# Kernel optimization log

Measured on AMD Instinct MI355X. Metric: run time of the kernel, lower is better.

The kernel has to match this reference:

```python
import jax, jax.numpy as jnp
import numpy as np

TILE = 128

def _dequant(Wq, scales, zeros):
    # Wq: [out, n_cols] int codes; scales/zeros: [n_tiles, out]
    n_cols = Wq.shape[1]
    tids = jnp.arange(n_cols) // TILE            # tile id per column
    s = scales[tids].T                           # [out, n_cols]
    z = zeros[tids].T                            # [out, n_cols]
    return (Wq.astype(jnp.float32) - z) * s

def setup_inputs() -> dict:
    key = jax.random.key(0)
    ks = jax.random.split(key, 9)
    B, IN, OUT = 256, 8192, 8192
    n_high, n_low = 2048, 6144
    nt_hi, nt_lo = 16, 48
    x = jax.random.normal(ks[0], (B, IN), dtype=jnp.float32)
    W_high_q = jax.random.randint(ks[1], (OUT, n_high), 0, 64, dtype=jnp.int32)
    W_low_q = jax.random.randint(ks[2], (OUT, n_low), 0, 32, dtype=jnp.int32)
    scales_high = jax.random.uniform(ks[3], (nt_hi, OUT), dtype=jnp.float32, minval=0.001, maxval=0.05)
    zeros_high = jax.random.normal(ks[4], (nt_hi, OUT), dtype=jnp.float32) * 16.0
    scales_low = jax.random.uniform(ks[5], (nt_lo, OUT), dtype=jnp.float32, minval=0.001, maxval=0.05)
    zeros_low = jax.random.normal(ks[6], (nt_lo, OUT), dtype=jnp.float32) * 8.0
    bias = jax.random.normal(ks[7], (OUT,), dtype=jnp.float32) * 0.02
    col_indices = jax.random.permutation(ks[8], IN).astype(jnp.int32)
    return {"x": x, "W_high_q": W_high_q, "W_low_q": W_low_q,
            "scales_high": scales_high, "zeros_high": zeros_high,
            "scales_low": scales_low, "zeros_low": zeros_low,
            "bias": bias, "col_indices": col_indices}

def reference(x, W_high_q, W_low_q, scales_high, zeros_high,
              scales_low, zeros_low, bias, col_indices):
    # Dequantize both precision regions (per-tile affine: (q - zero) * scale)
    W_high = _dequant(W_high_q, scales_high, zeros_high)   # [out, n_high]
    W_low = _dequant(W_low_q, scales_low, zeros_low)       # [out, n_low]
    W_perm = jnp.concatenate([W_high, W_low], axis=1)      # [out, in]
    # y = x @ W.T where W[:, col_indices] = W_perm  <=>  gather x columns instead
    x_perm = x[:, col_indices]                             # [B, in]
    return x_perm @ W_perm.T + bias[None, :]
```

## Files before the change

### kernel.cpp

```cpp
#include <hip/hip_runtime.h>
#include <stdint.h>


#define IN_DIM 8192
#define OUT_DIM 8192
#define BDIM 256
#define NH 2048
#define NL 6144
#define BN 64
#define BK 32
#define KSPLIT 4
#define KSEG (IN_DIM / KSPLIT)
#define NSTEP (KSEG / BK)
#define NTILE (KSEG / 128)

#define XOFF 0
#define WOFF 32768
#define SCOFF 40960
#define ZSOFF 45056

typedef __bf16 bf16x8 __attribute__((ext_vector_type(8)));
typedef float f32x4 __attribute__((ext_vector_type(4)));

__device__ __forceinline__ unsigned short bfbits(float f) {
  union { float f; unsigned int u; } v; v.f = f;
  unsigned int u = v.u;
  u += 0x7fffu + ((u >> 16) & 1u);
  return (unsigned short)(u >> 16);
}
__device__ __forceinline__ unsigned int pk2(float a, float b) {
  return (unsigned int)bfbits(a) | ((unsigned int)bfbits(b) << 16);
}

extern "C" __global__ void gather_k(const float* __restrict__ x,
                                    const int* __restrict__ ci,
                                    unsigned short* __restrict__ xp) {
  int i4 = blockIdx.x * blockDim.x + threadIdx.x;
  int b = i4 >> 11;
  int k4 = (i4 & 2047) << 2;
  int4 c = *(const int4*)(ci + k4);
  const float* xr = x + (size_t)b * IN_DIM;
  uint2 st;
  st.x = pk2(xr[c.x], xr[c.y]);
  st.y = pk2(xr[c.z], xr[c.w]);
  *(uint2*)(xp + (size_t)b * IN_DIM + k4) = st;
}

extern "C" __global__ __launch_bounds__(256, 2)
void gemm_k(const unsigned short* __restrict__ xp,
            const int* __restrict__ Whq, const int* __restrict__ Wlq,
            const float* __restrict__ sh, const float* __restrict__ zh,
            const float* __restrict__ sl, const float* __restrict__ zl,
            const float* __restrict__ bias,
            float* __restrict__ outp,
            int use_atomic)
{
  __shared__ char smem[49152];
  const int t = threadIdx.x;
  const int lane = t & 63;
  const int wv = t >> 6;
  const int kh = blockIdx.y;
  const int n0 = blockIdx.x * BN;
  const int l15 = lane & 15;
  const int g4 = lane >> 4;

  const int xr = t >> 2;
  const int xc = (t & 3) ^ (xr & 3);
  const unsigned short* xg0 = xp + (size_t)xr * IN_DIM + (size_t)kh * KSEG + xc * 8;

  const int wcol = t >> 2;
  const int wm = t & 3;
  const int* wb0 = (kh == 0) ? (Whq + (size_t)(n0 + wcol) * NH)
                             : (Wlq + (size_t)(n0 + wcol) * NL + (size_t)(kh - 1) * KSEG);
  const float* sbase = ((kh == 0) ? sh : sl + (size_t)(kh - 1) * NTILE * OUT_DIM) + n0;
  const float* zbase = ((kh == 0) ? zh : zl + (size_t)(kh - 1) * NTILE * OUT_DIM) + n0;

  f32x4 acc[4][4];
  {
    float bvj[4];
    #pragma unroll
    for (int j = 0; j < 4; ++j)
      bvj[j] = (kh == 0) ? bias[n0 + j * 16 + l15] : 0.f;
    #pragma unroll
    for (int i = 0; i < 4; ++i)
      #pragma unroll
      for (int j = 0; j < 4; ++j) {
        acc[i][j][0] = bvj[j]; acc[i][j][1] = bvj[j];
        acc[i][j][2] = bvj[j]; acc[i][j][3] = bvj[j];
      }
  }

  auto stage_x = [&](int bx, int s) {
    const unsigned short* g = xg0 + s * BK;
    char* lb = smem + XOFF + bx * 16384 + wv * 1024;
    #pragma unroll
    for (int r = 0; r < 4; ++r)
      __builtin_amdgcn_global_load_lds(
          (const __attribute__((address_space(1))) void*)(g + (size_t)r * 64 * IN_DIM),
          (__attribute__((address_space(3))) void*)(lb + r * 4096), 16, 0, 0);
  };
  auto wload = [&](int4& a, int4& b, int s) {
    const int* p = wb0 + s * BK + wm * 8;
    a = *(const int4*)p;
    b = *(const int4*)(p + 4);
  };
  auto wdeq = [&](int bx, int4 a, int4 b, int s) {
    int tl = s >> 2;
    float sc = *(const float*)(smem + SCOFF + (tl * 64 + wcol) * 4);
    float zs = *(const float*)(smem + ZSOFF + (tl * 64 + wcol) * 4);
    uint4 d;
    d.x = pk2((float)a.x * sc - zs, (float)a.y * sc - zs);
    d.y = pk2((float)a.z * sc - zs, (float)a.w * sc - zs);
    d.z = pk2((float)b.x * sc - zs, (float)b.y * sc - zs);
    d.w = pk2((float)b.z * sc - zs, (float)b.w * sc - zs);
    *(uint4*)(smem + WOFF + bx * 4096 + wcol * 64 + ((wm ^ (wcol & 3)) * 16)) = d;
  };
  auto compute = [&](int bx) {
    const char* xb = smem + XOFF + bx * 16384;
    const char* wbuf = smem + WOFF + bx * 4096;
    bf16x8 a[4], b[4];
    #pragma unroll
    for (int i = 0; i < 4; ++i) {
      int row = wv * 64 + i * 16 + l15;
      int ch = g4 ^ (row & 3);
      a[i] = *(const bf16x8*)(xb + row * 64 + ch * 16);
    }
    #pragma unroll
    for (int j = 0; j < 4; ++j) {
      int col = j * 16 + l15;
      int ch = g4 ^ (col & 3);
      b[j] = *(const bf16x8*)(wbuf + col * 64 + ch * 16);
    }
    #pragma unroll
    for (int i = 0; i < 4; ++i)
      #pragma unroll
      for (int j = 0; j < 4; ++j)
        acc[i][j] = __builtin_amdgcn_mfma_f32_16x16x32_bf16(a[i], b[j], acc[i][j], 0, 0, 0);
  };

  #pragma unroll
  for (int r = 0; r < 4; ++r) {
    int p = t + r * 256;
    float s_ = sbase[(size_t)(p >> 6) * OUT_DIM + (p & 63)];
    float z_ = zbase[(size_t)(p >> 6) * OUT_DIM + (p & 63)];
    *(float*)(smem + SCOFF + p * 4) = s_;
    *(float*)(smem + ZSOFF + p * 4) = z_ * s_;
  }
  stage_x(0, 0);
  int4 qa0, qa1, qb0, qb1;
  wload(qa0, qa1, 0);
  wload(qb0, qb1, 1);
  __syncthreads();
  wdeq(0, qa0, qa1, 0);
  asm volatile("s_waitcnt lgkmcnt(0)" ::: "memory");
  __builtin_amdgcn_s_barrier();

  #pragma unroll 1
  for (int it = 0; it < 31; ++it) {
    const int s = it * 2;
    __builtin_amdgcn_sched_barrier(0);
    stage_x(1, s + 1);
    __builtin_amdgcn_sched_barrier(0);
    wload(qa0, qa1, s + 2);
    __builtin_amdgcn_sched_barrier(0);
    compute(0);
    wdeq(1, qb0, qb1, s + 1);
    asm volatile("s_waitcnt vmcnt(2) lgkmcnt(0)" ::: "memory");
    __builtin_amdgcn_s_barrier();
    __builtin_amdgcn_sched_barrier(0);
    stage_x(0, s + 2);
    __builtin_amdgcn_sched_barrier(0);
    wload(qb0, qb1, s + 3);
    __builtin_amdgcn_sched_barrier(0);
    compute(1);
    wdeq(0, qa0, qa1, s + 2);
    asm volatile("s_waitcnt vmcnt(2) lgkmcnt(0)" ::: "memory");
    __builtin_amdgcn_s_barrier();
  }
  __builtin_amdgcn_sched_barrier(0);
  stage_x(1, 63);
  __builtin_amdgcn_sched_barrier(0);
  compute(0);
  wdeq(1, qb0, qb1, 63);
  asm volatile("s_waitcnt vmcnt(0) lgkmcnt(0)" ::: "memory");
  __builtin_amdgcn_s_barrier();
  compute(1);

  if (use_atomic) {
    #pragma unroll
    for (int i = 0; i < 4; ++i) {
      int row0 = wv * 64 + i * 16 + g4 * 4;
      #pragma unroll
      for (int j = 0; j < 4; ++j) {
        int col = n0 + j * 16 + l15;
        #pragma unroll
        for (int r = 0; r < 4; ++r)
          atomicAdd(&outp[(size_t)(row0 + r) * OUT_DIM + col], acc[i][j][r]);
      }
    }
  } else {
    float* pp = outp + (size_t)kh * ((size_t)BDIM * OUT_DIM);
    #pragma unroll
    for (int i = 0; i < 4; ++i) {
      int row0 = wv * 64 + i * 16 + g4 * 4;
      #pragma unroll
      for (int j = 0; j < 4; ++j) {
        int col = n0 + j * 16 + l15;
        #pragma unroll
        for (int r = 0; r < 4; ++r)
          pp[(size_t)(row0 + r) * OUT_DIM + col] = acc[i][j][r];
      }
    }
  }
}

extern "C" __global__ void reduce_k(const float* __restrict__ part,
                                    float* __restrict__ out) {
  int i4 = blockIdx.x * blockDim.x + threadIdx.x;
  size_t off = (size_t)i4 * 4;
  const size_t S = (size_t)BDIM * OUT_DIM;
  float4 p0 = *(const float4*)(part + off);
  float4 p1 = *(const float4*)(part + off + S);
  float4 p2 = *(const float4*)(part + off + 2 * S);
  float4 p3 = *(const float4*)(part + off + 3 * S);
  float4 r;
  r.x = p0.x + p1.x + p2.x + p3.x;
  r.y = p0.y + p1.y + p2.y + p3.y;
  r.z = p0.z + p1.z + p2.z + p3.z;
  r.w = p0.w + p1.w + p2.w + p3.w;
  *(float4*)(out + off) = r;
}

extern "C" void kernel_launch(void* const* d_in, const int* in_sizes, int n_in,
                              void* d_out, int out_size, void* d_ws, size_t ws_size,
                              hipStream_t stream) {
  const float* x   = (const float*)d_in[0];
  const int* Whq   = (const int*)d_in[1];
  const int* Wlq   = (const int*)d_in[2];
  const float* sh  = (const float*)d_in[3];
  const float* zh  = (const float*)d_in[4];
  const float* sl  = (const float*)d_in[5];
  const float* zl  = (const float*)d_in[6];
  const float* bias = (const float*)d_in[7];
  const int* ci    = (const int*)d_in[8];
  float* out = (float*)d_out;

  unsigned short* xp = (unsigned short*)d_ws;
  const size_t XP_BYTES = (size_t)BDIM * IN_DIM * 2;
  const size_t PART_BYTES = (size_t)KSPLIT * BDIM * OUT_DIM * 4;
  bool have_ws = ws_size >= XP_BYTES + PART_BYTES;

  gather_k<<<dim3(2048), dim3(256), 0, stream>>>(x, ci, xp);

  dim3 gg(OUT_DIM / BN, KSPLIT);
  if (have_ws) {
    float* part = (float*)((char*)d_ws + XP_BYTES);
    gemm_k<<<gg, dim3(256), 0, stream>>>(xp, Whq, Wlq, sh, zh, sl, zl, bias, part, 0);
    reduce_k<<<dim3(2048), dim3(256), 0, stream>>>(part, out);
  } else {
    hipMemsetAsync(d_out, 0, (size_t)out_size * sizeof(float), stream);
    gemm_k<<<gg, dim3(256), 0, stream>>>(xp, Whq, Wlq, sh, zh, sl, zl, bias, out, 1);
  }
}
```

Baseline: 388.1 us.

## Load activations directly to registers and deepen split-K with higher occupancy

Activation tiles are no longer staged through LDS. Each wave now loads its A fragments straight from global memory into registers, double-buffered across steps, which shrinks shared memory from 48KB to 16KB and raises the launch-bounds occupancy target from 2 to 4 blocks per CU. The kernel is templated on the split-K factor and uses 8 K-segments when the workspace allows, giving twice as many blocks, with a generic reduce over the partials. The risks are uncoalesced, row-strided direct global loads, and that the 8-way split doubles the partial-sum traffic written and read by the reduce.

```diff
diff --git a/kernel.cpp b/kernel.cpp
--- a/kernel.cpp
+++ b/kernel.cpp
@@ -9,15 +9,10 @@
 #define NL 6144
 #define BN 64
 #define BK 32
-#define KSPLIT 4
-#define KSEG (IN_DIM / KSPLIT)
-#define NSTEP (KSEG / BK)
-#define NTILE (KSEG / 128)
-
-#define XOFF 0
-#define WOFF 32768
-#define SCOFF 40960
-#define ZSOFF 45056
+
+#define WOFF 0
+#define SCOFF 8192
+#define ZSOFF 12288
 
 typedef __bf16 bf16x8 __attribute__((ext_vector_type(8)));
 typedef float f32x4 __attribute__((ext_vector_type(4)));
@@ -32,9 +27,9 @@
   return (unsigned int)bfbits(a) | ((unsigned int)bfbits(b) << 16);
 }
 
-extern "C" __global__ void gather_k(const float* __restrict__ x,
-                                    const int* __restrict__ ci,
-                                    unsigned short* __restrict__ xp) {
+__global__ void gather_k(const float* __restrict__ x,
+                         const int* __restrict__ ci,
+                         unsigned short* __restrict__ xp) {
   int i4 = blockIdx.x * blockDim.x + threadIdx.x;
   int b = i4 >> 11;
   int k4 = (i4 & 2047) << 2;
@@ -46,7 +41,8 @@
   *(uint2*)(xp + (size_t)b * IN_DIM + k4) = st;
 }
 
-extern "C" __global__ __launch_bounds__(256, 2)
+template<int KSPL>
+__global__ __launch_bounds__(256, 4)
 void gemm_k(const unsigned short* __restrict__ xp,
             const int* __restrict__ Whq, const int* __restrict__ Wlq,
             const float* __restrict__ sh, const float* __restrict__ zh,
@@ -55,7 +51,12 @@
             float* __restrict__ outp,
             int use_atomic)
 {
-  __shared__ char smem[49152];
+  constexpr int KSEG = IN_DIM / KSPL;
+  constexpr int NSTEP = KSEG / BK;
+  constexpr int NT = KSEG / 128;
+  constexpr int HSEG = NH / KSEG;
+
+  __shared__ char smem[16384];
   const int t = threadIdx.x;
   const int lane = t & 63;
   const int wv = t >> 6;
@@ -63,17 +64,19 @@
   const int n0 = blockIdx.x * BN;
   const int l15 = lane & 15;
   const int g4 = lane >> 4;
-
-  const int xr = t >> 2;
-  const int xc = (t & 3) ^ (xr & 3);
-  const unsigned short* xg0 = xp + (size_t)xr * IN_DIM + (size_t)kh * KSEG + xc * 8;
+  const bool hi = (kh < HSEG);
 
   const int wcol = t >> 2;
   const int wm = t & 3;
-  const int* wb0 = (kh == 0) ? (Whq + (size_t)(n0 + wcol) * NH)
-                             : (Wlq + (size_t)(n0 + wcol) * NL + (size_t)(kh - 1) * KSEG);
-  const float* sbase = ((kh == 0) ? sh : sl + (size_t)(kh - 1) * NTILE * OUT_DIM) + n0;
-  const float* zbase = ((kh == 0) ? zh : zl + (size_t)(kh - 1) * NTILE * OUT_DIM) + n0;
+  const int* wb0 = hi ? (Whq + (size_t)(n0 + wcol) * NH + (size_t)kh * KSEG)
+                      : (Wlq + (size_t)(n0 + wcol) * NL + (size_t)(kh - HSEG) * KSEG);
+  const float* sbase = (hi ? sh + (size_t)kh * NT * OUT_DIM
+                           : sl + (size_t)(kh - HSEG) * NT * OUT_DIM) + n0;
+  const float* zbase = (hi ? zh + (size_t)kh * NT * OUT_DIM
+                           : zl + (size_t)(kh - HSEG) * NT * OUT_DIM) + n0;
+
+  const unsigned short* xA = xp + (size_t)(wv * 64 + l15) * IN_DIM
+                                + (size_t)kh * KSEG + g4 * 8;
 
   f32x4 acc[4][4];
   {
@@ -90,14 +93,10 @@
       }
   }
 
-  auto stage_x = [&](int bx, int s) {
-    const unsigned short* g = xg0 + s * BK;
-    char* lb = smem + XOFF + bx * 16384 + wv * 1024;
-    #pragma unroll
-    for (int r = 0; r < 4; ++r)
-      __builtin_amdgcn_global_load_lds(
-          (const __attribute__((address_space(1))) void*)(g + (size_t)r * 64 * IN_DIM),
-          (__attribute__((address_space(3))) void*)(lb + r * 4096), 16, 0, 0);
+  auto aload = [&](bf16x8 (&af)[4], int s) {
+    #pragma unroll
+    for (int i = 0; i < 4; ++i)
+      af[i] = *(const bf16x8*)(xA + (size_t)i * 16 * IN_DIM + s * BK);
   };
   auto wload = [&](int4& a, int4& b, int s) {
     const int* p = wb0 + s * BK + wm * 8;
@@ -115,16 +114,9 @@
     d.w = pk2((float)b.z * sc - zs, (float)b.w * sc - zs);
     *(uint4*)(smem + WOFF + bx * 4096 + wcol * 64 + ((wm ^ (wcol & 3)) * 16)) = d;
   };
-  auto compute = [&](int bx) {
-    const char* xb = smem + XOFF + bx * 16384;
+  auto compute = [&](int bx, const bf16x8 (&af)[4]) {
     const char* wbuf = smem + WOFF + bx * 4096;
-    bf16x8 a[4], b[4];
-    #pragma unroll
-    for (int i = 0; i < 4; ++i) {
-      int row = wv * 64 + i * 16 + l15;
-      int ch = g4 ^ (row & 3);
-      a[i] = *(const bf16x8*)(xb + row * 64 + ch * 16);
-    }
+    bf16x8 b[4];
     #pragma unroll
     for (int j = 0; j < 4; ++j) {
       int col = j * 16 + l15;
@@ -135,56 +127,57 @@
     for (int i = 0; i < 4; ++i)
       #pragma unroll
       for (int j = 0; j < 4; ++j)
-        acc[i][j] = __builtin_amdgcn_mfma_f32_16x16x32_bf16(a[i], b[j], acc[i][j], 0, 0, 0);
+        acc[i][j] = __builtin_amdgcn_mfma_f32_16x16x32_bf16(af[i], b[j], acc[i][j], 0, 0, 0);
   };
 
   #pragma unroll
-  for (int r = 0; r < 4; ++r) {
-    int p = t + r * 256;
+  for (int r = 0; r < (NT * 64) / BDIM; ++r) {
+    int p = t + r * BDIM;
     float s_ = sbase[(size_t)(p >> 6) * OUT_DIM + (p & 63)];
     float z_ = zbase[(size_t)(p >> 6) * OUT_DIM + (p & 63)];
     *(float*)(smem + SCOFF + p * 4) = s_;
     *(float*)(smem + ZSOFF + p * 4) = z_ * s_;
   }
-  stage_x(0, 0);
+  __syncthreads();
+
+  bf16x8 afA[4], afB[4];
   int4 qa0, qa1, qb0, qb1;
+  aload(afA, 0);
   wload(qa0, qa1, 0);
   wload(qb0, qb1, 1);
-  __syncthreads();
   wdeq(0, qa0, qa1, 0);
-  asm volatile("s_waitcnt lgkmcnt(0)" ::: "memory");
+  asm volatile("s_waitcnt lgkmcnt(0)");
+  __builtin_amdgcn_sched_barrier(0);
   __builtin_amdgcn_s_barrier();
 
   #pragma unroll 1
-  for (int it = 0; it < 31; ++it) {
+  for (int it = 0; it < NSTEP / 2 - 1; ++it) {
     const int s = it * 2;
-    __builtin_amdgcn_sched_barrier(0);
-    stage_x(1, s + 1);
-    __builtin_amdgcn_sched_barrier(0);
+    aload(afB, s + 1);
     wload(qa0, qa1, s + 2);
     __builtin_amdgcn_sched_barrier(0);
-    compute(0);
     wdeq(1, qb0, qb1, s + 1);
-    asm volatile("s_waitcnt vmcnt(2) lgkmcnt(0)" ::: "memory");
+    compute(0, afA);
+    asm volatile("s_waitcnt lgkmcnt(0)");
+    __builtin_amdgcn_sched_barrier(0);
     __builtin_amdgcn_s_barrier();
-    __builtin_amdgcn_sched_barrier(0);
-    stage_x(0, s + 2);
-    __builtin_amdgcn_sched_barrier(0);
+    aload(afA, s + 2);
     wload(qb0, qb1, s + 3);
     __builtin_amdgcn_sched_barrier(0);
-    compute(1);
     wdeq(0, qa0, qa1, s + 2);
-    asm volatile("s_waitcnt vmcnt(2) lgkmcnt(0)" ::: "memory");
+    compute(1, afB);
+    asm volatile("s_waitcnt lgkmcnt(0)");
+    __builtin_amdgcn_sched_barrier(0);
     __builtin_amdgcn_s_barrier();
   }
+  aload(afB, NSTEP - 1);
   __builtin_amdgcn_sched_barrier(0);
-  stage_x(1, 63);
+  wdeq(1, qb0, qb1, NSTEP - 1);
+  compute(0, afA);
+  asm volatile("s_waitcnt lgkmcnt(0)");
   __builtin_amdgcn_sched_barrier(0);
-  compute(0);
-  wdeq(1, qb0, qb1, 63);
-  asm volatile("s_waitcnt vmcnt(0) lgkmcnt(0)" ::: "memory");
   __builtin_amdgcn_s_barrier();
-  compute(1);
+  compute(1, afB);
 
   if (use_atomic) {
     #pragma unroll
@@ -214,20 +207,18 @@
   }
 }
 
-extern "C" __global__ void reduce_k(const float* __restrict__ part,
-                                    float* __restrict__ out) {
+template<int NS>
+__global__ void reduce_k(const float* __restrict__ part,
+                         float* __restrict__ out) {
   int i4 = blockIdx.x * blockDim.x + threadIdx.x;
   size_t off = (size_t)i4 * 4;
   const size_t S = (size_t)BDIM * OUT_DIM;
-  float4 p0 = *(const float4*)(part + off);
-  float4 p1 = *(const float4*)(part + off + S);
-  float4 p2 = *(const float4*)(part + off + 2 * S);
-  float4 p3 = *(const float4*)(part + off + 3 * S);
-  float4 r;
-  r.x = p0.x + p1.x + p2.x + p3.x;
-  r.y = p0.y + p1.y + p2.y + p3.y;
-  r.z = p0.z + p1.z + p2.z + p3.z;
-  r.w = p0.w + p1.w + p2.w + p3.w;
+  float4 r = *(const float4*)(part + off);
+  #pragma unroll
+  for (int k = 1; k < NS; ++k) {
+    float4 p = *(const float4*)(part + off + (size_t)k * S);
+    r.x += p.x; r.y += p.y; r.z += p.z; r.w += p.w;
+  }
   *(float4*)(out + off) = r;
 }
 
@@ -247,18 +238,25 @@
 
   unsigned short* xp = (unsigned short*)d_ws;
   const size_t XP_BYTES = (size_t)BDIM * IN_DIM * 2;
-  const size_t PART_BYTES = (size_t)KSPLIT * BDIM * OUT_DIM * 4;
-  bool have_ws = ws_size >= XP_BYTES + PART_BYTES;
+  const size_t SEG_BYTES = (size_t)BDIM * OUT_DIM * 4;
+  bool ws8 = ws_size >= XP_BYTES + 8 * SEG_BYTES;
+  bool ws4 = ws_size >= XP_BYTES + 4 * SEG_BYTES;
 
   gather_k<<<dim3(2048), dim3(256), 0, stream>>>(x, ci, xp);
 
-  dim3 gg(OUT_DIM / BN, KSPLIT);
-  if (have_ws) {
+  if (ws8) {
     float* part = (float*)((char*)d_ws + XP_BYTES);
-    gemm_k<<<gg, dim3(256), 0, stream>>>(xp, Whq, Wlq, sh, zh, sl, zl, bias, part, 0);
-    reduce_k<<<dim3(2048), dim3(256), 0, stream>>>(part, out);
+    gemm_k<8><<<dim3(OUT_DIM / BN, 8), dim3(256), 0, stream>>>(
+        xp, Whq, Wlq, sh, zh, sl, zl, bias, part, 0);
+    reduce_k<8><<<dim3(2048), dim3(256), 0, stream>>>(part, out);
+  } else if (ws4) {
+    float* part = (float*)((char*)d_ws + XP_BYTES);
+    gemm_k<4><<<dim3(OUT_DIM / BN, 4), dim3(256), 0, stream>>>(
+        xp, Whq, Wlq, sh, zh, sl, zl, bias, part, 0);
+    reduce_k<4><<<dim3(2048), dim3(256), 0, stream>>>(part, out);
   } else {
     hipMemsetAsync(d_out, 0, (size_t)out_size * sizeof(float), stream);
-    gemm_k<<<gg, dim3(256), 0, stream>>>(xp, Whq, Wlq, sh, zh, sl, zl, bias, out, 1);
-  }
-}
+    gemm_k<4><<<dim3(OUT_DIM / BN, 4), dim3(256), 0, stream>>>(
+        xp, Whq, Wlq, sh, zh, sl, zl, bias, out, 1);
+  }
+}
```

Measured after the change: 465.6 us. 1.2x slower.

## Stream raw int weights to LDS asynchronously and dequantize at MFMA operand load

Applied to the files above, without the earlier changes.

Weight codes are now copied straight into LDS with global_load_lds through a 4-deep ring buffer instead of going through registers, and are dequantized to bf16 right before the MFMA. This drops the separate register-side dequant-and-store stage. The N tile shrinks from 64 to 32 to fit LDS and raise occupancy to 3 blocks per CU. The grid is flattened with a swizzled block-to-tile mapping so that neighbouring blocks share x segments. In exchange, each wave now dequantizes per compute step (4x redundant across waves), there is less MFMA work per block, and total x traffic goes up because of the smaller tile.

```diff
diff --git a/kernel.cpp b/kernel.cpp
--- a/kernel.cpp
+++ b/kernel.cpp
@@ -7,17 +7,17 @@
 #define BDIM 256
 #define NH 2048
 #define NL 6144
-#define BN 64
+#define BN 32
 #define BK 32
 #define KSPLIT 4
-#define KSEG (IN_DIM / KSPLIT)
-#define NSTEP (KSEG / BK)
-#define NTILE (KSEG / 128)
+#define KSEG 2048
+#define NSTEP 64
+#define NT 16
 
 #define XOFF 0
 #define WOFF 32768
-#define SCOFF 40960
-#define ZSOFF 45056
+#define SCOFF 49152
+#define ZSOFF 51200
 
 typedef __bf16 bf16x8 __attribute__((ext_vector_type(8)));
 typedef float f32x4 __attribute__((ext_vector_type(4)));
@@ -32,9 +32,9 @@
   return (unsigned int)bfbits(a) | ((unsigned int)bfbits(b) << 16);
 }
 
-extern "C" __global__ void gather_k(const float* __restrict__ x,
-                                    const int* __restrict__ ci,
-                                    unsigned short* __restrict__ xp) {
+__global__ void gather_k(const float* __restrict__ x,
+                         const int* __restrict__ ci,
+                         unsigned short* __restrict__ xp) {
   int i4 = blockIdx.x * blockDim.x + threadIdx.x;
   int b = i4 >> 11;
   int k4 = (i4 & 2047) << 2;
@@ -46,7 +46,7 @@
   *(uint2*)(xp + (size_t)b * IN_DIM + k4) = st;
 }
 
-extern "C" __global__ __launch_bounds__(256, 2)
+__global__ __launch_bounds__(256, 3)
 void gemm_k(const unsigned short* __restrict__ xp,
             const int* __restrict__ Whq, const int* __restrict__ Wlq,
             const float* __restrict__ sh, const float* __restrict__ zh,
@@ -55,143 +55,161 @@
             float* __restrict__ outp,
             int use_atomic)
 {
-  __shared__ char smem[49152];
+  __shared__ char smem[53248];
   const int t = threadIdx.x;
   const int lane = t & 63;
   const int wv = t >> 6;
-  const int kh = blockIdx.y;
-  const int n0 = blockIdx.x * BN;
   const int l15 = lane & 15;
   const int g4 = lane >> 4;
 
-  const int xr = t >> 2;
-  const int xc = (t & 3) ^ (xr & 3);
-  const unsigned short* xg0 = xp + (size_t)xr * IN_DIM + (size_t)kh * KSEG + xc * 8;
-
-  const int wcol = t >> 2;
-  const int wm = t & 3;
-  const int* wb0 = (kh == 0) ? (Whq + (size_t)(n0 + wcol) * NH)
-                             : (Wlq + (size_t)(n0 + wcol) * NL + (size_t)(kh - 1) * KSEG);
-  const float* sbase = ((kh == 0) ? sh : sl + (size_t)(kh - 1) * NTILE * OUT_DIM) + n0;
-  const float* zbase = ((kh == 0) ? zh : zl + (size_t)(kh - 1) * NTILE * OUT_DIM) + n0;
-
-  f32x4 acc[4][4];
+  const int swz = (blockIdx.x & 7) * 128 + (blockIdx.x >> 3);
+  const int kh = swz >> 8;
+  const int n0 = (swz & 255) * BN;
+  const bool hi = (kh == 0);
+
+  const int xrow = t >> 2;
+  const unsigned short* xsrc0 = xp + (size_t)xrow * IN_DIM + (size_t)kh * KSEG
+                                   + ((t & 3) ^ (xrow & 3)) * 8;
+  const int wcol = t >> 3;
+  const int* wsrc0 = (hi ? Whq + (size_t)(n0 + wcol) * NH
+                         : Wlq + (size_t)(n0 + wcol) * NL + (size_t)(kh - 1) * KSEG)
+                     + ((t & 7) ^ (wcol & 7)) * 4;
+
+  const float* sb = (hi ? sh : sl + (size_t)(kh - 1) * NT * OUT_DIM) + n0;
+  const float* zb = (hi ? zh : zl + (size_t)(kh - 1) * NT * OUT_DIM) + n0;
+
+  f32x4 acc[4][2];
   {
-    float bvj[4];
-    #pragma unroll
-    for (int j = 0; j < 4; ++j)
-      bvj[j] = (kh == 0) ? bias[n0 + j * 16 + l15] : 0.f;
-    #pragma unroll
-    for (int i = 0; i < 4; ++i)
-      #pragma unroll
-      for (int j = 0; j < 4; ++j) {
-        acc[i][j][0] = bvj[j]; acc[i][j][1] = bvj[j];
-        acc[i][j][2] = bvj[j]; acc[i][j][3] = bvj[j];
-      }
-  }
-
-  auto stage_x = [&](int bx, int s) {
-    const unsigned short* g = xg0 + s * BK;
-    char* lb = smem + XOFF + bx * 16384 + wv * 1024;
+    float bv0 = hi ? bias[n0 + l15] : 0.f;
+    float bv1 = hi ? bias[n0 + 16 + l15] : 0.f;
+    #pragma unroll
+    for (int i = 0; i < 4; ++i) {
+      acc[i][0][0] = bv0; acc[i][0][1] = bv0; acc[i][0][2] = bv0; acc[i][0][3] = bv0;
+      acc[i][1][0] = bv1; acc[i][1][1] = bv1; acc[i][1][2] = bv1; acc[i][1][3] = bv1;
+    }
+  }
+
+  auto stage_x = [&](int s) {
+    const unsigned short* g = xsrc0 + s * BK;
+    char* lb = smem + XOFF + (s & 1) * 16384 + wv * 1024;
     #pragma unroll
     for (int r = 0; r < 4; ++r)
       __builtin_amdgcn_global_load_lds(
           (const __attribute__((address_space(1))) void*)(g + (size_t)r * 64 * IN_DIM),
           (__attribute__((address_space(3))) void*)(lb + r * 4096), 16, 0, 0);
   };
-  auto wload = [&](int4& a, int4& b, int s) {
-    const int* p = wb0 + s * BK + wm * 8;
-    a = *(const int4*)p;
-    b = *(const int4*)(p + 4);
-  };
-  auto wdeq = [&](int bx, int4 a, int4 b, int s) {
-    int tl = s >> 2;
-    float sc = *(const float*)(smem + SCOFF + (tl * 64 + wcol) * 4);
-    float zs = *(const float*)(smem + ZSOFF + (tl * 64 + wcol) * 4);
-    uint4 d;
-    d.x = pk2((float)a.x * sc - zs, (float)a.y * sc - zs);
-    d.y = pk2((float)a.z * sc - zs, (float)a.w * sc - zs);
-    d.z = pk2((float)b.x * sc - zs, (float)b.y * sc - zs);
-    d.w = pk2((float)b.z * sc - zs, (float)b.w * sc - zs);
-    *(uint4*)(smem + WOFF + bx * 4096 + wcol * 64 + ((wm ^ (wcol & 3)) * 16)) = d;
-  };
-  auto compute = [&](int bx) {
-    const char* xb = smem + XOFF + bx * 16384;
-    const char* wbuf = smem + WOFF + bx * 4096;
-    bf16x8 a[4], b[4];
+  auto stage_w = [&](int s) {
+    __builtin_amdgcn_global_load_lds(
+        (const __attribute__((address_space(1))) void*)(wsrc0 + s * BK),
+        (__attribute__((address_space(3))) void*)(smem + WOFF + (s & 3) * 4096 + wv * 1024),
+        16, 0, 0);
+  };
+  auto dq8 = [&](int4 a, int4 b, float sc, float zs) -> bf16x8 {
+    bf16x8 r;
+    r[0] = (__bf16)((float)a.x * sc - zs);
+    r[1] = (__bf16)((float)a.y * sc - zs);
+    r[2] = (__bf16)((float)a.z * sc - zs);
+    r[3] = (__bf16)((float)a.w * sc - zs);
+    r[4] = (__bf16)((float)b.x * sc - zs);
+    r[5] = (__bf16)((float)b.y * sc - zs);
+    r[6] = (__bf16)((float)b.z * sc - zs);
+    r[7] = (__bf16)((float)b.w * sc - zs);
+    return r;
+  };
+  auto rdsc = [&](int tl, int j, float& sc, float& zs) {
+    int idx = (tl * 32 + j * 16 + l15) * 4;
+    sc = *(const float*)(smem + SCOFF + idx);
+    zs = *(const float*)(smem + ZSOFF + idx);
+  };
+  auto compute = [&](const char* xb, const char* wb,
+                     float sc0, float zs0, float sc1, float zs1) {
+    bf16x8 a[4];
     #pragma unroll
     for (int i = 0; i < 4; ++i) {
       int row = wv * 64 + i * 16 + l15;
-      int ch = g4 ^ (row & 3);
-      a[i] = *(const bf16x8*)(xb + row * 64 + ch * 16);
-    }
-    #pragma unroll
-    for (int j = 0; j < 4; ++j) {
-      int col = j * 16 + l15;
-      int ch = g4 ^ (col & 3);
-      b[j] = *(const bf16x8*)(wbuf + col * 64 + ch * 16);
-    }
-    #pragma unroll
-    for (int i = 0; i < 4; ++i)
-      #pragma unroll
-      for (int j = 0; j < 4; ++j)
-        acc[i][j] = __builtin_amdgcn_mfma_f32_16x16x32_bf16(a[i], b[j], acc[i][j], 0, 0, 0);
+      a[i] = *(const bf16x8*)(xb + row * 64 + (g4 ^ (row & 3)) * 16);
+    }
+    int c0 = l15, c1 = 16 + l15;
+    const char* b0p = wb + c0 * 128;
+    const char* b1p = wb + c1 * 128;
+    int4 w0 = *(const int4*)(b0p + ((2 * g4) ^ (c0 & 7)) * 16);
+    int4 w1 = *(const int4*)(b0p + ((2 * g4 + 1) ^ (c0 & 7)) * 16);
+    int4 v0 = *(const int4*)(b1p + ((2 * g4) ^ (c1 & 7)) * 16);
+    int4 v1 = *(const int4*)(b1p + ((2 * g4 + 1) ^ (c1 & 7)) * 16);
+    bf16x8 b0 = dq8(w0, w1, sc0, zs0);
+    bf16x8 b1 = dq8(v0, v1, sc1, zs1);
+    #pragma unroll
+    for (int i = 0; i < 4; ++i) {
+      acc[i][0] = __builtin_amdgcn_mfma_f32_16x16x32_bf16(a[i], b0, acc[i][0], 0, 0, 0);
+      acc[i][1] = __builtin_amdgcn_mfma_f32_16x16x32_bf16(a[i], b1, acc[i][1], 0, 0, 0);
+    }
   };
 
   #pragma unroll
-  for (int r = 0; r < 4; ++r) {
+  for (int r = 0; r < 2; ++r) {
     int p = t + r * 256;
-    float s_ = sbase[(size_t)(p >> 6) * OUT_DIM + (p & 63)];
-    float z_ = zbase[(size_t)(p >> 6) * OUT_DIM + (p & 63)];
+    float s_ = sb[(size_t)(p >> 5) * OUT_DIM + (p & 31)];
+    float z_ = zb[(size_t)(p >> 5) * OUT_DIM + (p & 31)];
     *(float*)(smem + SCOFF + p * 4) = s_;
     *(float*)(smem + ZSOFF + p * 4) = z_ * s_;
   }
-  stage_x(0, 0);
-  int4 qa0, qa1, qb0, qb1;
-  wload(qa0, qa1, 0);
-  wload(qb0, qb1, 1);
   __syncthreads();
-  wdeq(0, qa0, qa1, 0);
-  asm volatile("s_waitcnt lgkmcnt(0)" ::: "memory");
+  stage_x(0);
+  stage_w(0); stage_w(1); stage_w(2);
+  __builtin_amdgcn_sched_barrier(0);
+  asm volatile("s_waitcnt vmcnt(2)");
+  __builtin_amdgcn_sched_barrier(0);
   __builtin_amdgcn_s_barrier();
 
   #pragma unroll 1
-  for (int it = 0; it < 31; ++it) {
-    const int s = it * 2;
-    __builtin_amdgcn_sched_barrier(0);
-    stage_x(1, s + 1);
-    __builtin_amdgcn_sched_barrier(0);
-    wload(qa0, qa1, s + 2);
-    __builtin_amdgcn_sched_barrier(0);
-    compute(0);
-    wdeq(1, qb0, qb1, s + 1);
-    asm volatile("s_waitcnt vmcnt(2) lgkmcnt(0)" ::: "memory");
+  for (int it = 0; it < 15; ++it) {
+    float sc0, zs0, sc1, zs1;
+    rdsc(it, 0, sc0, zs0);
+    rdsc(it, 1, sc1, zs1);
+    #pragma unroll
+    for (int d = 0; d < 4; ++d) {
+      const int s = it * 4 + d;
+      stage_x(s + 1);
+      stage_w(s + 3);
+      compute(smem + XOFF + (d & 1) * 16384, smem + WOFF + d * 4096,
+              sc0, zs0, sc1, zs1);
+      __builtin_amdgcn_sched_barrier(0);
+      asm volatile("s_waitcnt vmcnt(1)");
+      __builtin_amdgcn_sched_barrier(0);
+      __builtin_amdgcn_s_barrier();
+    }
+  }
+  {
+    float sc0, zs0, sc1, zs1;
+    rdsc(15, 0, sc0, zs0);
+    rdsc(15, 1, sc1, zs1);
+    stage_x(61); stage_w(63);
+    compute(smem + XOFF + 0, smem + WOFF + 0, sc0, zs0, sc1, zs1);
+    __builtin_amdgcn_sched_barrier(0);
+    asm volatile("s_waitcnt vmcnt(1)");
+    __builtin_amdgcn_sched_barrier(0);
     __builtin_amdgcn_s_barrier();
-    __builtin_amdgcn_sched_barrier(0);
-    stage_x(0, s + 2);
-    __builtin_amdgcn_sched_barrier(0);
-    wload(qb0, qb1, s + 3);
-    __builtin_amdgcn_sched_barrier(0);
-    compute(1);
-    wdeq(0, qa0, qa1, s + 2);
-    asm volatile("s_waitcnt vmcnt(2) lgkmcnt(0)" ::: "memory");
+    stage_x(62);
+    compute(smem + XOFF + 16384, smem + WOFF + 4096, sc0, zs0, sc1, zs1);
+    __builtin_amdgcn_sched_barrier(0);
+    asm volatile("s_waitcnt vmcnt(0)");
+    __builtin_amdgcn_sched_barrier(0);
     __builtin_amdgcn_s_barrier();
-  }
-  __builtin_amdgcn_sched_barrier(0);
-  stage_x(1, 63);
-  __builtin_amdgcn_sched_barrier(0);
-  compute(0);
-  wdeq(1, qb0, qb1, 63);
-  asm volatile("s_waitcnt vmcnt(0) lgkmcnt(0)" ::: "memory");
-  __builtin_amdgcn_s_barrier();
-  compute(1);
+    stage_x(63);
+    compute(smem + XOFF + 0, smem + WOFF + 8192, sc0, zs0, sc1, zs1);
+    __builtin_amdgcn_sched_barrier(0);
+    asm volatile("s_waitcnt vmcnt(0)");
+    __builtin_amdgcn_sched_barrier(0);
+    __builtin_amdgcn_s_barrier();
+    compute(smem + XOFF + 16384, smem + WOFF + 12288, sc0, zs0, sc1, zs1);
+  }
 
   if (use_atomic) {
     #pragma unroll
     for (int i = 0; i < 4; ++i) {
       int row0 = wv * 64 + i * 16 + g4 * 4;
       #pragma unroll
-      for (int j = 0; j < 4; ++j) {
+      for (int j = 0; j < 2; ++j) {
         int col = n0 + j * 16 + l15;
         #pragma unroll
         for (int r = 0; r < 4; ++r)
@@ -204,7 +222,7 @@
     for (int i = 0; i < 4; ++i) {
       int row0 = wv * 64 + i * 16 + g4 * 4;
       #pragma unroll
-      for (int j = 0; j < 4; ++j) {
+      for (int j = 0; j < 2; ++j) {
         int col = n0 + j * 16 + l15;
         #pragma unroll
         for (int r = 0; r < 4; ++r)
@@ -214,8 +232,8 @@
   }
 }
 
-extern "C" __global__ void reduce_k(const float* __restrict__ part,
-                                    float* __restrict__ out) {
+__global__ void reduce_k(const float* __restrict__ part,
+                         float* __restrict__ out) {
   int i4 = blockIdx.x * blockDim.x + threadIdx.x;
   size_t off = (size_t)i4 * 4;
   const size_t S = (size_t)BDIM * OUT_DIM;
@@ -252,7 +270,7 @@
 
   gather_k<<<dim3(2048), dim3(256), 0, stream>>>(x, ci, xp);
 
-  dim3 gg(OUT_DIM / BN, KSPLIT);
+  dim3 gg(KSPLIT * (OUT_DIM / BN));
   if (have_ws) {
     float* part = (float*)((char*)d_ws + XP_BYTES);
     gemm_k<<<gg, dim3(256), 0, stream>>>(xp, Whq, Wlq, sh, zh, sl, zl, bias, part, 0);
```

Result: slower. 506.8 us (+30.6%).
